# Kernel tuning notes

Hardware: AMD Instinct MI355X
Metric: run time of the kernel (lower is better)

## Reference

```python
import jax, jax.numpy as jnp
import numpy as np

B, H, S, O = 16384, 512, 6, 1


def setup_inputs() -> dict:
    key = jax.random.key(0)
    ks = jax.random.split(key, 14)
    w = lambda k, shape: jax.random.normal(k, shape, dtype=jnp.float32) * 0.02
    return {
        "input": jax.random.normal(ks[0], (B, O), dtype=jnp.float32),
        "hidden": jax.random.normal(ks[1], (B, H), dtype=jnp.float32),
        "cell": jax.random.normal(ks[2], (B, H), dtype=jnp.float32),
        "encoder_outputs": jax.random.normal(ks[3], (B, S, H), dtype=jnp.float32),
        # attn: Linear(2H+O -> S)
        "W_attn": w(ks[4], (S, 2 * H + O)),
        "b_attn": w(ks[5], (S,)),
        # attn_combine: Linear(H+O -> H)
        "W_comb": w(ks[6], (H, H + O)),
        "b_comb": w(ks[7], (H,)),
        # LSTM(H -> H), torch gate order i,f,g,o
        "W_ih": w(ks[8], (4 * H, H)),
        "W_hh": w(ks[9], (4 * H, H)),
        "b_ih": w(ks[10], (4 * H,)),
        "b_hh": w(ks[11], (4 * H,)),
        # out: Linear(H -> O)
        "W_out": w(ks[12], (O, H)),
        "b_out": w(ks[13], (O,)),
    }


def reference(input, hidden, cell, encoder_outputs,
              W_attn, b_attn, W_comb, b_comb,
              W_ih, W_hh, b_ih, b_hh, W_out, b_out):
    # Bahdanau-style attention over encoder outputs (eval mode: dropout = identity)
    attn_in = jnp.concatenate([input, hidden, cell], axis=1)          # [B, 2H+O]
    attn_weights = jax.nn.softmax(attn_in @ W_attn.T + b_attn, axis=1)  # [B, S]
    attn_applied = jnp.einsum("bs,bsh->bh", attn_weights, encoder_outputs)  # [B, H]

    x = jnp.concatenate([input, attn_applied], axis=1)                # [B, H+O]
    x = jax.nn.relu(x @ W_comb.T + b_comb)                            # [B, H]

    # single LSTM step (torch gate order: i, f, g, o)
    gates = x @ W_ih.T + b_ih + hidden @ W_hh.T + b_hh               # [B, 4H]
    i, f, g, o = jnp.split(gates, 4, axis=1)
    c_new = jax.nn.sigmoid(f) * cell + jax.nn.sigmoid(i) * jnp.tanh(g)
    h_new = jax.nn.sigmoid(o) * jnp.tanh(c_new)

    output = h_new @ W_out.T + b_out                                  # [B, O]
    return output, h_new, c_new, attn_weights[:, None, :]
```

## Files before the change

### kernel.cpp

```cpp
#include <hip/hip_runtime.h>
#include <hip/hip_bf16.h>

typedef __attribute__((ext_vector_type(8))) short frag8;
typedef __attribute__((ext_vector_type(4))) float f32x4;

#define ASYNC16(gsrc, ldst) \
  __builtin_amdgcn_global_load_lds((const __attribute__((address_space(1))) void*)(gsrc), \
                                   (__attribute__((address_space(3))) void*)(ldst), 16, 0, 0)

__device__ __forceinline__ float sigmoid_(float x) { return 1.0f / (1.0f + __expf(-x)); }
__device__ __forceinline__ float tanh_(float x)    { return 1.0f - 2.0f / (__expf(2.0f * x) + 1.0f); }

__global__ __launch_bounds__(256) void prep_kernel(
    const float* __restrict__ W_comb, const float* __restrict__ W_ih,
    const float* __restrict__ W_hh, const float* __restrict__ b_ih,
    const float* __restrict__ b_hh,
    __hip_bfloat16* __restrict__ Wc, __hip_bfloat16* __restrict__ Wg,
    float* __restrict__ biasg)
{
  int idx = blockIdx.x * 256 + threadIdx.x;
  const int NW = 2048 * 1024, NC = 512 * 512;
  if (idx < NW) {
    int np = idx >> 10, k = idx & 1023;
    int j = (np >> 4) & 3;
    int u = ((np >> 6) << 4) | (np & 15);
    int n = j * 512 + u;
    float v = (k < 512) ? W_ih[n * 512 + k] : W_hh[n * 512 + (k - 512)];
    Wg[idx] = __float2bfloat16(v);
  } else if (idx < NW + NC) {
    int t = idx - NW;
    int n = t >> 9, k = t & 511;
    Wc[t] = __float2bfloat16(W_comb[n * 513 + 1 + k]);
  } else if (idx < NW + NC + 2048) {
    int np = idx - NW - NC;
    int j = (np >> 4) & 3;
    int u = ((np >> 6) << 4) | (np & 15);
    int n = j * 512 + u;
    biasg[np] = b_ih[n] + b_hh[n];
  }
}

__global__ __launch_bounds__(256) void attn_kernel(
    const float* __restrict__ inputv, const float* __restrict__ hidden,
    const float* __restrict__ cell, const float* __restrict__ enc,
    const float* __restrict__ W_attn, const float* __restrict__ b_attn,
    __hip_bfloat16* __restrict__ A1, __hip_bfloat16* __restrict__ Z,
    float* __restrict__ outA)
{
  __shared__ float Wlh[6 * 1024];
  __shared__ float Wl0[6];
  const int tid = threadIdx.x;
  for (int i = tid; i < 6 * 1024; i += 256) {
    int s = i >> 10, k = i & 1023;
    Wlh[i] = W_attn[s * 1025 + 1 + k];
  }
  if (tid < 6) Wl0[tid] = W_attn[tid * 1025];
  __syncthreads();
  const int w = tid >> 6, lane = tid & 63;
  const long row = (long)blockIdx.x * 4 + w;
  const int k8 = lane * 8;

  const float4* hp4 = (const float4*)(hidden + row * 512 + k8);
  const float4* cp4 = (const float4*)(cell + row * 512 + k8);
  float4 h0 = hp4[0], h1 = hp4[1];
  float4 c0 = cp4[0], c1 = cp4[1];

  float acc[6];
#pragma unroll
  for (int s = 0; s < 6; ++s) {
    const float4* wh = (const float4*)(Wlh + s * 1024 + k8);
    const float4* wc = (const float4*)(Wlh + s * 1024 + 512 + k8);
    float4 a0 = wh[0], a1 = wh[1], b0 = wc[0], b1 = wc[1];
    acc[s] = h0.x * a0.x + h0.y * a0.y + h0.z * a0.z + h0.w * a0.w
           + h1.x * a1.x + h1.y * a1.y + h1.z * a1.z + h1.w * a1.w
           + c0.x * b0.x + c0.y * b0.y + c0.z * b0.z + c0.w * b0.w
           + c1.x * b1.x + c1.y * b1.y + c1.z * b1.z + c1.w * b1.w;
  }
  float iv = inputv[row];
  float logit[6];
#pragma unroll
  for (int s = 0; s < 6; ++s) {
    float a = acc[s];
#pragma unroll
    for (int d = 32; d > 0; d >>= 1) a += __shfl_xor(a, d);
    logit[s] = a + iv * Wl0[s] + b_attn[s];
  }
  float mx = logit[0];
#pragma unroll
  for (int s = 1; s < 6; ++s) mx = fmaxf(mx, logit[s]);
  float wts[6], tot = 0.f;
#pragma unroll
  for (int s = 0; s < 6; ++s) { wts[s] = __expf(logit[s] - mx); tot += wts[s]; }
  float rt = 1.f / tot;
#pragma unroll
  for (int s = 0; s < 6; ++s) wts[s] *= rt;
  if (lane < 6) {
    float mw = 0.f;
#pragma unroll
    for (int s = 0; s < 6; ++s) if (lane == s) mw = wts[s];
    outA[row * 6 + lane] = mw;
  }
  float a8[8] = {0.f, 0.f, 0.f, 0.f, 0.f, 0.f, 0.f, 0.f};
  const float* ep = enc + row * 3072 + k8;
#pragma unroll
  for (int s = 0; s < 6; ++s) {
    float4 e0 = *(const float4*)(ep + s * 512);
    float4 e1 = *(const float4*)(ep + s * 512 + 4);
    float ws_ = wts[s];
    a8[0] += ws_ * e0.x; a8[1] += ws_ * e0.y; a8[2] += ws_ * e0.z; a8[3] += ws_ * e0.w;
    a8[4] += ws_ * e1.x; a8[5] += ws_ * e1.y; a8[6] += ws_ * e1.z; a8[7] += ws_ * e1.w;
  }
  union { frag8 v; __hip_bfloat16 h[8]; } pa, ph;
  float hv8[8] = {h0.x, h0.y, h0.z, h0.w, h1.x, h1.y, h1.z, h1.w};
#pragma unroll
  for (int i = 0; i < 8; ++i) { pa.h[i] = __float2bfloat16(a8[i]); ph.h[i] = __float2bfloat16(hv8[i]); }
  *(frag8*)(A1 + row * 512 + k8) = pa.v;
  *(frag8*)(Z + row * 1024 + 512 + k8) = ph.v;
}

__device__ __forceinline__ void stage16(const __hip_bfloat16* __restrict__ g, int ld,
                                        int row0, int k0, __hip_bfloat16* lds, int tid)
{
  int c0 = tid, c1 = tid + 256;
  const __hip_bfloat16* g0 = g + (long)(row0 + (c0 >> 2)) * ld + k0 + (c0 & 3) * 8;
  const __hip_bfloat16* g1 = g + (long)(row0 + (c1 >> 2)) * ld + k0 + (c1 & 3) * 8;
  char* l0 = (char*)lds + (tid & ~63) * 16;
  ASYNC16(g0, l0);
  ASYNC16(g1, l0 + 4096);
}

__global__ __launch_bounds__(256) void comb_gemm(
    const __hip_bfloat16* __restrict__ A, const __hip_bfloat16* __restrict__ Bt,
    const float* __restrict__ b_comb, const float* __restrict__ W_comb,
    const float* __restrict__ inputv, __hip_bfloat16* __restrict__ Z)
{
  __shared__ __align__(16) __hip_bfloat16 As[2][128 * 32];
  __shared__ __align__(16) __hip_bfloat16 Bs[2][128 * 32];
  const int tid = threadIdx.x;
  const int lane = tid & 63, w = tid >> 6;
  const int quad = lane >> 4, l15 = lane & 15;
  const int m0 = blockIdx.y * 128, n0 = blockIdx.x * 128;
  const int wm = (w & 1) * 64, wn = (w >> 1) * 64;

  f32x4 acc[4][4] = {};
  for (int kt = 0; kt < 8; ++kt) {
    int k0 = kt * 64;
    stage16(A, 512, m0, k0, As[0], tid);
    stage16(A, 512, m0, k0 + 32, As[1], tid);
    stage16(Bt, 512, n0, k0, Bs[0], tid);
    stage16(Bt, 512, n0, k0 + 32, Bs[1], tid);
    __syncthreads();
#pragma unroll
    for (int h = 0; h < 2; ++h) {
      frag8 af[4], bf[4];
#pragma unroll
      for (int i = 0; i < 4; ++i)
        af[i] = *(const frag8*)((const short*)As[h] + (wm + i * 16 + l15) * 32 + quad * 8);
#pragma unroll
      for (int j = 0; j < 4; ++j)
        bf[j] = *(const frag8*)((const short*)Bs[h] + (wn + j * 16 + l15) * 32 + quad * 8);
#pragma unroll
      for (int i = 0; i < 4; ++i)
#pragma unroll
        for (int j = 0; j < 4; ++j)
          acc[i][j] = __builtin_amdgcn_mfma_f32_16x16x32_bf16(af[i], bf[j], acc[i][j], 0, 0, 0);
    }
    __syncthreads();
  }
  float bc[4], w0[4];
#pragma unroll
  for (int j = 0; j < 4; ++j) {
    int col = n0 + wn + j * 16 + l15;
    bc[j] = b_comb[col];
    w0[j] = W_comb[col * 513];
  }
#pragma unroll
  for (int i = 0; i < 4; ++i) {
#pragma unroll
    for (int r = 0; r < 4; ++r) {
      int row = m0 + wm + i * 16 + quad * 4 + r;
      float iv = inputv[row];
#pragma unroll
      for (int j = 0; j < 4; ++j) {
        int col = n0 + wn + j * 16 + l15;
        float v = acc[i][j][r] + bc[j] + iv * w0[j];
        Z[(long)row * 1024 + col] = __float2bfloat16(fmaxf(v, 0.0f));
      }
    }
  }
}

__global__ __launch_bounds__(256) void gates_gemm(
    const __hip_bfloat16* __restrict__ Zm, const __hip_bfloat16* __restrict__ Wg,
    const float* __restrict__ biasg, const float* __restrict__ cell,
    float* __restrict__ outH, float* __restrict__ outC)
{
  __shared__ __align__(16) __hip_bfloat16 As[2][128 * 32];
  __shared__ __align__(16) __hip_bfloat16 Bs[2][128 * 32];
  const int tid = threadIdx.x;
  const int lane = tid & 63, w = tid >> 6;
  const int quad = lane >> 4, l15 = lane & 15;
  const int m0 = blockIdx.y * 128, n0 = blockIdx.x * 128;
  const int wm = (w & 1) * 64, wn = (w >> 1) * 64;

  f32x4 acc[4][4] = {};
  for (int kt = 0; kt < 16; ++kt) {
    int k0 = kt * 64;
    stage16(Zm, 1024, m0, k0, As[0], tid);
    stage16(Zm, 1024, m0, k0 + 32, As[1], tid);
    stage16(Wg, 1024, n0, k0, Bs[0], tid);
    stage16(Wg, 1024, n0, k0 + 32, Bs[1], tid);
    __syncthreads();
#pragma unroll
    for (int h = 0; h < 2; ++h) {
      frag8 af[4], bf[4];
#pragma unroll
      for (int i = 0; i < 4; ++i)
        af[i] = *(const frag8*)((const short*)As[h] + (wm + i * 16 + l15) * 32 + quad * 8);
#pragma unroll
      for (int j = 0; j < 4; ++j)
        bf[j] = *(const frag8*)((const short*)Bs[h] + (wn + j * 16 + l15) * 32 + quad * 8);
#pragma unroll
      for (int i = 0; i < 4; ++i)
#pragma unroll
        for (int j = 0; j < 4; ++j)
          acc[i][j] = __builtin_amdgcn_mfma_f32_16x16x32_bf16(af[i], bf[j], acc[i][j], 0, 0, 0);
    }
    __syncthreads();
  }
  const int u = ((n0 + wn) >> 2) + l15;
  const float bi = biasg[n0 + wn + l15];
  const float bfg = biasg[n0 + wn + 16 + l15];
  const float bgg = biasg[n0 + wn + 32 + l15];
  const float bo = biasg[n0 + wn + 48 + l15];
#pragma unroll
  for (int i = 0; i < 4; ++i) {
#pragma unroll
    for (int r = 0; r < 4; ++r) {
      long row = m0 + wm + i * 16 + quad * 4 + r;
      float cv = cell[row * 512 + u];
      float ig = acc[i][0][r] + bi;
      float fg = acc[i][1][r] + bfg;
      float gg = acc[i][2][r] + bgg;
      float og = acc[i][3][r] + bo;
      float cn = sigmoid_(fg) * cv + sigmoid_(ig) * tanh_(gg);
      float hn = sigmoid_(og) * tanh_(cn);
      outH[row * 512 + u] = hn;
      outC[row * 512 + u] = cn;
    }
  }
}

__global__ __launch_bounds__(256) void out_gemv(
    const float* __restrict__ h, const float* __restrict__ W_out,
    const float* __restrict__ b_out, float* __restrict__ out)
{
  __shared__ float wl[512];
  const int tid = threadIdx.x;
  for (int i = tid; i < 512; i += 256) wl[i] = W_out[i];
  __syncthreads();
  const int w = tid >> 6, lane = tid & 63;
  const long row = (long)blockIdx.x * 4 + w;
  const int k8 = lane * 8;
  const float4* hp4 = (const float4*)(h + row * 512 + k8);
  const float4* wp4 = (const float4*)(wl + k8);
  float4 h0 = hp4[0], h1 = hp4[1];
  float4 w0 = wp4[0], w1 = wp4[1];
  float s = h0.x * w0.x + h0.y * w0.y + h0.z * w0.z + h0.w * w0.w
          + h1.x * w1.x + h1.y * w1.y + h1.z * w1.z + h1.w * w1.w;
#pragma unroll
  for (int d = 32; d > 0; d >>= 1) s += __shfl_xor(s, d);
  if (lane == 0) out[row] = s + b_out[0];
}

extern "C" void kernel_launch(void* const* d_in, const int* in_sizes, int n_in,
                              void* d_out, int out_size, void* d_ws, size_t ws_size,
                              hipStream_t stream) {
  const float* inputv = (const float*)d_in[0];
  const float* hidden = (const float*)d_in[1];
  const float* cell   = (const float*)d_in[2];
  const float* enc    = (const float*)d_in[3];
  const float* W_attn = (const float*)d_in[4];
  const float* b_attn = (const float*)d_in[5];
  const float* W_comb = (const float*)d_in[6];
  const float* b_comb = (const float*)d_in[7];
  const float* W_ih   = (const float*)d_in[8];
  const float* W_hh   = (const float*)d_in[9];
  const float* b_ih   = (const float*)d_in[10];
  const float* b_hh   = (const float*)d_in[11];
  const float* W_out  = (const float*)d_in[12];
  const float* b_out  = (const float*)d_in[13];

  float* out  = (float*)d_out;
  float* outO = out;
  float* outH = out + 16384;
  float* outC = out + 8404992;
  float* outA = out + 16793600;

  char* ws = (char*)d_ws;
  __hip_bfloat16* Z   = (__hip_bfloat16*)ws;
  __hip_bfloat16* A1  = (__hip_bfloat16*)(ws + 33554432);
  __hip_bfloat16* Wc  = (__hip_bfloat16*)(ws + 50331648);
  __hip_bfloat16* Wg  = (__hip_bfloat16*)(ws + 50855936);
  float*          bg  = (float*)(ws + 55050240);

  prep_kernel<<<9224, 256, 0, stream>>>(W_comb, W_ih, W_hh, b_ih, b_hh, Wc, Wg, bg);
  attn_kernel<<<4096, 256, 0, stream>>>(inputv, hidden, cell, enc, W_attn, b_attn, A1, Z, outA);
  comb_gemm<<<dim3(4, 128), 256, 0, stream>>>(A1, Wc, b_comb, W_comb, inputv, Z);
  gates_gemm<<<dim3(16, 128), 256, 0, stream>>>(Z, Wg, bg, cell, outH, outC);
  out_gemv<<<4096, 256, 0, stream>>>(outH, W_out, b_out, outO);
}
```

Measured before the change: 503.9 us.

## Fuse output GEMV into gates GEMM, enlarge tiles, batch attention rows per block

The separate out_gemv kernel is removed. Its dot product is now done in the gates GEMM epilogue through a shuffle reduction and atomicAdd into an output that prep_kernel fills with b_out. The gates GEMM M tile doubles to 256 with launch_bounds(256,2), and both GEMMs swap grid axes so consecutive blocks walk M. The attention kernel runs 512 threads that handle 8 rows per wave, with a padded LDS layout for the attention weights. The atomics make the summation order nondeterministic, and the larger tile raises register pressure.

New measurement: 511.2 us. No clear change (+1.5%).

```diff
diff --git a/kernel.cpp b/kernel.cpp
--- a/kernel.cpp
+++ b/kernel.cpp
@@ -14,9 +14,9 @@
 __global__ __launch_bounds__(256) void prep_kernel(
     const float* __restrict__ W_comb, const float* __restrict__ W_ih,
     const float* __restrict__ W_hh, const float* __restrict__ b_ih,
-    const float* __restrict__ b_hh,
+    const float* __restrict__ b_hh, const float* __restrict__ b_out,
     __hip_bfloat16* __restrict__ Wc, __hip_bfloat16* __restrict__ Wg,
-    float* __restrict__ biasg)
+    float* __restrict__ biasg, float* __restrict__ outO)
 {
   int idx = blockIdx.x * 256 + threadIdx.x;
   const int NW = 2048 * 1024, NC = 512 * 512;
@@ -37,89 +37,95 @@
     int u = ((np >> 6) << 4) | (np & 15);
     int n = j * 512 + u;
     biasg[np] = b_ih[n] + b_hh[n];
-  }
-}
-
-__global__ __launch_bounds__(256) void attn_kernel(
+  } else if (idx < NW + NC + 2048 + 16384) {
+    outO[idx - NW - NC - 2048] = b_out[0];
+  }
+}
+
+__global__ __launch_bounds__(512) void attn_kernel(
     const float* __restrict__ inputv, const float* __restrict__ hidden,
     const float* __restrict__ cell, const float* __restrict__ enc,
     const float* __restrict__ W_attn, const float* __restrict__ b_attn,
     __hip_bfloat16* __restrict__ A1, __hip_bfloat16* __restrict__ Z,
     float* __restrict__ outA)
 {
-  __shared__ float Wlh[6 * 1024];
+  __shared__ float Wl[6 * 1152];
   __shared__ float Wl0[6];
   const int tid = threadIdx.x;
-  for (int i = tid; i < 6 * 1024; i += 256) {
+  for (int i = tid; i < 6 * 1024; i += 512) {
     int s = i >> 10, k = i & 1023;
-    Wlh[i] = W_attn[s * 1025 + 1 + k];
+    Wl[s * 1152 + k + ((k >> 5) << 2)] = W_attn[s * 1025 + 1 + k];
   }
   if (tid < 6) Wl0[tid] = W_attn[tid * 1025];
   __syncthreads();
   const int w = tid >> 6, lane = tid & 63;
-  const long row = (long)blockIdx.x * 4 + w;
   const int k8 = lane * 8;
-
-  const float4* hp4 = (const float4*)(hidden + row * 512 + k8);
-  const float4* cp4 = (const float4*)(cell + row * 512 + k8);
-  float4 h0 = hp4[0], h1 = hp4[1];
-  float4 c0 = cp4[0], c1 = cp4[1];
-
-  float acc[6];
-#pragma unroll
-  for (int s = 0; s < 6; ++s) {
-    const float4* wh = (const float4*)(Wlh + s * 1024 + k8);
-    const float4* wc = (const float4*)(Wlh + s * 1024 + 512 + k8);
-    float4 a0 = wh[0], a1 = wh[1], b0 = wc[0], b1 = wc[1];
-    acc[s] = h0.x * a0.x + h0.y * a0.y + h0.z * a0.z + h0.w * a0.w
-           + h1.x * a1.x + h1.y * a1.y + h1.z * a1.z + h1.w * a1.w
-           + c0.x * b0.x + c0.y * b0.y + c0.z * b0.z + c0.w * b0.w
-           + c1.x * b1.x + c1.y * b1.y + c1.z * b1.z + c1.w * b1.w;
-  }
-  float iv = inputv[row];
-  float logit[6];
-#pragma unroll
-  for (int s = 0; s < 6; ++s) {
-    float a = acc[s];
-#pragma unroll
-    for (int d = 32; d > 0; d >>= 1) a += __shfl_xor(a, d);
-    logit[s] = a + iv * Wl0[s] + b_attn[s];
-  }
-  float mx = logit[0];
-#pragma unroll
-  for (int s = 1; s < 6; ++s) mx = fmaxf(mx, logit[s]);
-  float wts[6], tot = 0.f;
-#pragma unroll
-  for (int s = 0; s < 6; ++s) { wts[s] = __expf(logit[s] - mx); tot += wts[s]; }
-  float rt = 1.f / tot;
-#pragma unroll
-  for (int s = 0; s < 6; ++s) wts[s] *= rt;
-  if (lane < 6) {
-    float mw = 0.f;
-#pragma unroll
-    for (int s = 0; s < 6; ++s) if (lane == s) mw = wts[s];
-    outA[row * 6 + lane] = mw;
-  }
-  float a8[8] = {0.f, 0.f, 0.f, 0.f, 0.f, 0.f, 0.f, 0.f};
-  const float* ep = enc + row * 3072 + k8;
-#pragma unroll
-  for (int s = 0; s < 6; ++s) {
-    float4 e0 = *(const float4*)(ep + s * 512);
-    float4 e1 = *(const float4*)(ep + s * 512 + 4);
-    float ws_ = wts[s];
-    a8[0] += ws_ * e0.x; a8[1] += ws_ * e0.y; a8[2] += ws_ * e0.z; a8[3] += ws_ * e0.w;
-    a8[4] += ws_ * e1.x; a8[5] += ws_ * e1.y; a8[6] += ws_ * e1.z; a8[7] += ws_ * e1.w;
-  }
-  union { frag8 v; __hip_bfloat16 h[8]; } pa, ph;
-  float hv8[8] = {h0.x, h0.y, h0.z, h0.w, h1.x, h1.y, h1.z, h1.w};
-#pragma unroll
-  for (int i = 0; i < 8; ++i) { pa.h[i] = __float2bfloat16(a8[i]); ph.h[i] = __float2bfloat16(hv8[i]); }
-  *(frag8*)(A1 + row * 512 + k8) = pa.v;
-  *(frag8*)(Z + row * 1024 + 512 + k8) = ph.v;
-}
-
-__device__ __forceinline__ void stage16(const __hip_bfloat16* __restrict__ g, int ld,
-                                        int row0, int k0, __hip_bfloat16* lds, int tid)
+  const int idx0 = k8 + ((k8 >> 5) << 2);
+  const int idxc = idx0 + 576;
+
+  for (int rr = 0; rr < 8; ++rr) {
+    const long row = (long)blockIdx.x * 64 + w * 8 + rr;
+    const float4* hp4 = (const float4*)(hidden + row * 512 + k8);
+    const float4* cp4 = (const float4*)(cell + row * 512 + k8);
+    float4 h0 = hp4[0], h1 = hp4[1];
+    float4 c0 = cp4[0], c1 = cp4[1];
+
+    float acc[6];
+#pragma unroll
+    for (int s = 0; s < 6; ++s) {
+      const float4* wh = (const float4*)(Wl + s * 1152 + idx0);
+      const float4* wc = (const float4*)(Wl + s * 1152 + idxc);
+      float4 a0 = wh[0], a1 = wh[1], b0 = wc[0], b1 = wc[1];
+      acc[s] = h0.x * a0.x + h0.y * a0.y + h0.z * a0.z + h0.w * a0.w
+             + h1.x * a1.x + h1.y * a1.y + h1.z * a1.z + h1.w * a1.w
+             + c0.x * b0.x + c0.y * b0.y + c0.z * b0.z + c0.w * b0.w
+             + c1.x * b1.x + c1.y * b1.y + c1.z * b1.z + c1.w * b1.w;
+    }
+    float iv = inputv[row];
+    float logit[6];
+#pragma unroll
+    for (int s = 0; s < 6; ++s) {
+      float a = acc[s];
+#pragma unroll
+      for (int d = 32; d > 0; d >>= 1) a += __shfl_xor(a, d);
+      logit[s] = a + iv * Wl0[s] + b_attn[s];
+    }
+    float mx = logit[0];
+#pragma unroll
+    for (int s = 1; s < 6; ++s) mx = fmaxf(mx, logit[s]);
+    float wts[6], tot = 0.f;
+#pragma unroll
+    for (int s = 0; s < 6; ++s) { wts[s] = __expf(logit[s] - mx); tot += wts[s]; }
+    float rt = 1.f / tot;
+#pragma unroll
+    for (int s = 0; s < 6; ++s) wts[s] *= rt;
+    if (lane < 6) {
+      float mw = 0.f;
+#pragma unroll
+      for (int s = 0; s < 6; ++s) if (lane == s) mw = wts[s];
+      outA[row * 6 + lane] = mw;
+    }
+    float a8[8] = {0.f, 0.f, 0.f, 0.f, 0.f, 0.f, 0.f, 0.f};
+    const float* ep = enc + row * 3072 + k8;
+#pragma unroll
+    for (int s = 0; s < 6; ++s) {
+      float4 e0 = *(const float4*)(ep + s * 512);
+      float4 e1 = *(const float4*)(ep + s * 512 + 4);
+      float ws_ = wts[s];
+      a8[0] += ws_ * e0.x; a8[1] += ws_ * e0.y; a8[2] += ws_ * e0.z; a8[3] += ws_ * e0.w;
+      a8[4] += ws_ * e1.x; a8[5] += ws_ * e1.y; a8[6] += ws_ * e1.z; a8[7] += ws_ * e1.w;
+    }
+    union { frag8 v; __hip_bfloat16 h[8]; } pa, ph;
+    float hv8[8] = {h0.x, h0.y, h0.z, h0.w, h1.x, h1.y, h1.z, h1.w};
+#pragma unroll
+    for (int i = 0; i < 8; ++i) { pa.h[i] = __float2bfloat16(a8[i]); ph.h[i] = __float2bfloat16(hv8[i]); }
+    *(frag8*)(A1 + row * 512 + k8) = pa.v;
+    *(frag8*)(Z + row * 1024 + 512 + k8) = ph.v;
+  }
+}
+
+__device__ __forceinline__ void stageB(const __hip_bfloat16* __restrict__ g, int ld,
+                                       int row0, int k0, __hip_bfloat16* lds, int tid)
 {
   int c0 = tid, c1 = tid + 256;
   const __hip_bfloat16* g0 = g + (long)(row0 + (c0 >> 2)) * ld + k0 + (c0 & 3) * 8;
@@ -129,6 +135,18 @@
   ASYNC16(g1, l0 + 4096);
 }
 
+__device__ __forceinline__ void stageA256(const __hip_bfloat16* __restrict__ g, int ld,
+                                          int row0, int k0, __hip_bfloat16* lds, int tid)
+{
+  char* l0 = (char*)lds + (tid & ~63) * 16;
+#pragma unroll
+  for (int t = 0; t < 4; ++t) {
+    int c = tid + t * 256;
+    const __hip_bfloat16* gp = g + (long)(row0 + (c >> 2)) * ld + k0 + (c & 3) * 8;
+    ASYNC16(gp, l0 + t * 4096);
+  }
+}
+
 __global__ __launch_bounds__(256) void comb_gemm(
     const __hip_bfloat16* __restrict__ A, const __hip_bfloat16* __restrict__ Bt,
     const float* __restrict__ b_comb, const float* __restrict__ W_comb,
@@ -139,16 +157,16 @@
   const int tid = threadIdx.x;
   const int lane = tid & 63, w = tid >> 6;
   const int quad = lane >> 4, l15 = lane & 15;
-  const int m0 = blockIdx.y * 128, n0 = blockIdx.x * 128;
+  const int m0 = blockIdx.x * 128, n0 = blockIdx.y * 128;
   const int wm = (w & 1) * 64, wn = (w >> 1) * 64;
 
   f32x4 acc[4][4] = {};
   for (int kt = 0; kt < 8; ++kt) {
     int k0 = kt * 64;
-    stage16(A, 512, m0, k0, As[0], tid);
-    stage16(A, 512, m0, k0 + 32, As[1], tid);
-    stage16(Bt, 512, n0, k0, Bs[0], tid);
-    stage16(Bt, 512, n0, k0 + 32, Bs[1], tid);
+    stageB(A, 512, m0, k0, As[0], tid);
+    stageB(A, 512, m0, k0 + 32, As[1], tid);
+    stageB(Bt, 512, n0, k0, Bs[0], tid);
+    stageB(Bt, 512, n0, k0 + 32, Bs[1], tid);
     __syncthreads();
 #pragma unroll
     for (int h = 0; h < 2; ++h) {
@@ -190,51 +208,52 @@
   }
 }
 
-__global__ __launch_bounds__(256) void gates_gemm(
+__global__ __launch_bounds__(256, 2) void gates_gemm(
     const __hip_bfloat16* __restrict__ Zm, const __hip_bfloat16* __restrict__ Wg,
     const float* __restrict__ biasg, const float* __restrict__ cell,
-    float* __restrict__ outH, float* __restrict__ outC)
-{
-  __shared__ __align__(16) __hip_bfloat16 As[2][128 * 32];
+    const float* __restrict__ W_out,
+    float* __restrict__ outH, float* __restrict__ outC, float* __restrict__ outO)
+{
+  __shared__ __align__(16) __hip_bfloat16 As[2][256 * 32];
   __shared__ __align__(16) __hip_bfloat16 Bs[2][128 * 32];
   const int tid = threadIdx.x;
   const int lane = tid & 63, w = tid >> 6;
   const int quad = lane >> 4, l15 = lane & 15;
-  const int m0 = blockIdx.y * 128, n0 = blockIdx.x * 128;
-  const int wm = (w & 1) * 64, wn = (w >> 1) * 64;
-
-  f32x4 acc[4][4] = {};
+  const int m0 = blockIdx.x * 256, n0 = blockIdx.y * 128;
+  const int wm = (w & 1) * 128, wn = (w >> 1) * 64;
+
+  f32x4 acc[8][4] = {};
   for (int kt = 0; kt < 16; ++kt) {
     int k0 = kt * 64;
-    stage16(Zm, 1024, m0, k0, As[0], tid);
-    stage16(Zm, 1024, m0, k0 + 32, As[1], tid);
-    stage16(Wg, 1024, n0, k0, Bs[0], tid);
-    stage16(Wg, 1024, n0, k0 + 32, Bs[1], tid);
+    stageA256(Zm, 1024, m0, k0, As[0], tid);
+    stageA256(Zm, 1024, m0, k0 + 32, As[1], tid);
+    stageB(Wg, 1024, n0, k0, Bs[0], tid);
+    stageB(Wg, 1024, n0, k0 + 32, Bs[1], tid);
     __syncthreads();
 #pragma unroll
     for (int h = 0; h < 2; ++h) {
-      frag8 af[4], bf[4];
-#pragma unroll
-      for (int i = 0; i < 4; ++i)
-        af[i] = *(const frag8*)((const short*)As[h] + (wm + i * 16 + l15) * 32 + quad * 8);
+      frag8 bf[4];
 #pragma unroll
       for (int j = 0; j < 4; ++j)
         bf[j] = *(const frag8*)((const short*)Bs[h] + (wn + j * 16 + l15) * 32 + quad * 8);
 #pragma unroll
-      for (int i = 0; i < 4; ++i)
+      for (int i = 0; i < 8; ++i) {
+        frag8 af = *(const frag8*)((const short*)As[h] + (wm + i * 16 + l15) * 32 + quad * 8);
 #pragma unroll
         for (int j = 0; j < 4; ++j)
-          acc[i][j] = __builtin_amdgcn_mfma_f32_16x16x32_bf16(af[i], bf[j], acc[i][j], 0, 0, 0);
+          acc[i][j] = __builtin_amdgcn_mfma_f32_16x16x32_bf16(af, bf[j], acc[i][j], 0, 0, 0);
+      }
     }
     __syncthreads();
   }
   const int u = ((n0 + wn) >> 2) + l15;
+  const float wout = W_out[u];
   const float bi = biasg[n0 + wn + l15];
   const float bfg = biasg[n0 + wn + 16 + l15];
   const float bgg = biasg[n0 + wn + 32 + l15];
   const float bo = biasg[n0 + wn + 48 + l15];
 #pragma unroll
-  for (int i = 0; i < 4; ++i) {
+  for (int i = 0; i < 8; ++i) {
 #pragma unroll
     for (int r = 0; r < 4; ++r) {
       long row = m0 + wm + i * 16 + quad * 4 + r;
@@ -247,30 +266,12 @@
       float hn = sigmoid_(og) * tanh_(cn);
       outH[row * 512 + u] = hn;
       outC[row * 512 + u] = cn;
-    }
-  }
-}
-
-__global__ __launch_bounds__(256) void out_gemv(
-    const float* __restrict__ h, const float* __restrict__ W_out,
-    const float* __restrict__ b_out, float* __restrict__ out)
-{
-  __shared__ float wl[512];
-  const int tid = threadIdx.x;
-  for (int i = tid; i < 512; i += 256) wl[i] = W_out[i];
-  __syncthreads();
-  const int w = tid >> 6, lane = tid & 63;
-  const long row = (long)blockIdx.x * 4 + w;
-  const int k8 = lane * 8;
-  const float4* hp4 = (const float4*)(h + row * 512 + k8);
-  const float4* wp4 = (const float4*)(wl + k8);
-  float4 h0 = hp4[0], h1 = hp4[1];
-  float4 w0 = wp4[0], w1 = wp4[1];
-  float s = h0.x * w0.x + h0.y * w0.y + h0.z * w0.z + h0.w * w0.w
-          + h1.x * w1.x + h1.y * w1.y + h1.z * w1.z + h1.w * w1.w;
-#pragma unroll
-  for (int d = 32; d > 0; d >>= 1) s += __shfl_xor(s, d);
-  if (lane == 0) out[row] = s + b_out[0];
+      float p = hn * wout;
+      p += __shfl_xor(p, 1); p += __shfl_xor(p, 2);
+      p += __shfl_xor(p, 4); p += __shfl_xor(p, 8);
+      if (l15 == 0) atomicAdd(outO + row, p);
+    }
+  }
 }
 
 extern "C" void kernel_launch(void* const* d_in, const int* in_sizes, int n_in,
@@ -304,9 +305,8 @@
   __hip_bfloat16* Wg  = (__hip_bfloat16*)(ws + 50855936);
   float*          bg  = (float*)(ws + 55050240);
 
-  prep_kernel<<<9224, 256, 0, stream>>>(W_comb, W_ih, W_hh, b_ih, b_hh, Wc, Wg, bg);
-  attn_kernel<<<4096, 256, 0, stream>>>(inputv, hidden, cell, enc, W_attn, b_attn, A1, Z, outA);
-  comb_gemm<<<dim3(4, 128), 256, 0, stream>>>(A1, Wc, b_comb, W_comb, inputv, Z);
-  gates_gemm<<<dim3(16, 128), 256, 0, stream>>>(Z, Wg, bg, cell, outH, outC);
-  out_gemv<<<4096, 256, 0, stream>>>(outH, W_out, b_out, outO);
-}
+  prep_kernel<<<9288, 256, 0, stream>>>(W_comb, W_ih, W_hh, b_ih, b_hh, b_out, Wc, Wg, bg, outO);
+  attn_kernel<<<256, 512, 0, stream>>>(inputv, hidden, cell, enc, W_attn, b_attn, A1, Z, outA);
+  comb_gemm<<<dim3(128, 4), 256, 0, stream>>>(A1, Wc, b_comb, W_comb, inputv, Z);
+  gates_gemm<<<dim3(64, 16), 256, 0, stream>>>(Z, Wg, bg, cell, W_out, outH, outC, outO);
+}
```
